# Performance work log

Measured on AMD Instinct MI355X. Metric: run time of the kernel, lower is better.

The kernel has to match this reference:

```python
import jax, jax.numpy as jnp
import numpy as np

B, T, E, H = 2, 2048, 768, 12
DH = E // H  # per-head attention dim
EPS = 1e-5


def setup_inputs() -> dict:
    key = jax.random.key(0)
    ks = jax.random.split(key, 12)
    s = 0.02
    return {
        "x": jax.random.normal(ks[0], (B, T, E), dtype=jnp.float32),
        # stacked per-head projection weights: [H, E, DH], biases [H, DH]
        "Wq": jax.random.normal(ks[1], (H, E, DH), dtype=jnp.float32) * s,
        "bq": jax.random.normal(ks[2], (H, DH), dtype=jnp.float32) * s,
        "Wk": jax.random.normal(ks[3], (H, E, DH), dtype=jnp.float32) * s,
        "bk": jax.random.normal(ks[4], (H, DH), dtype=jnp.float32) * s,
        "Wv": jax.random.normal(ks[5], (H, E, DH), dtype=jnp.float32) * s,
        "bv": jax.random.normal(ks[6], (H, DH), dtype=jnp.float32) * s,
        "Wo": jax.random.normal(ks[7], (E, E), dtype=jnp.float32) * s,
        "bo": jax.random.normal(ks[8], (E,), dtype=jnp.float32) * s,
        "gamma": jnp.ones((E,), dtype=jnp.float32),
        "beta": jnp.zeros((E,), dtype=jnp.float32),
    }


def reference(x, Wq, bq, Wk, bk, Wv, bv, Wo, bo, gamma, beta):
    # per-head projections (heads stacked on axis h)
    q = jnp.einsum("bte,hed->bhtd", x, Wq) + bq[None, :, None, :]
    k = jnp.einsum("bte,hed->bhtd", x, Wk) + bk[None, :, None, :]
    v = jnp.einsum("bte,hed->bhtd", x, Wv) + bv[None, :, None, :]

    scores = jnp.einsum("bhtd,bhsd->bhts", q, k) / jnp.sqrt(jnp.float32(DH))
    causal = jnp.tril(jnp.ones((T, T), dtype=bool))  # True = keep
    scores = jnp.where(causal[None, None], scores, -jnp.inf)
    attn = jax.nn.softmax(scores, axis=-1)
    o = jnp.einsum("bhts,bhsd->bhtd", attn, v)  # [B,H,T,DH]

    # concat heads in head order -> [B,T,E]
    concat = jnp.transpose(o, (0, 2, 1, 3)).reshape(B, T, E)
    proj = concat @ Wo + bo

    # LayerNorm(proj) then residual add
    mu = jnp.mean(proj, axis=-1, keepdims=True)
    var = jnp.mean((proj - mu) ** 2, axis=-1, keepdims=True)
    normed = (proj - mu) * jax.lax.rsqrt(var + EPS) * gamma + beta
    return x + normed
```

## Files before the change

kernel.cpp:

```cpp
#include <hip/hip_runtime.h>
#include <stdint.h>

#define NROWS 4096
#define EMB   768
#define NQKV  2304
#define TSEQ  2048
#define NHEAD 12
#define NBH   24

typedef unsigned short u16;
typedef u16  ushort4v __attribute__((ext_vector_type(4)));
typedef u16  ushort8 __attribute__((ext_vector_type(8)));
typedef __bf16 bf16x8 __attribute__((ext_vector_type(8)));
typedef float f32x4 __attribute__((ext_vector_type(4)));

typedef const __attribute__((address_space(1))) void* gas_ptr;
typedef __attribute__((address_space(3))) void* las_ptr;

__device__ __forceinline__ u16 f2bf(float f) {
  union { float f; uint32_t u; } v; v.f = f;
  uint32_t u = v.u;
  return (u16)((u + 0x7fffu + ((u >> 16) & 1u)) >> 16);
}
__device__ __forceinline__ float bf2f(u16 u) {
  union { uint32_t u; float f; } v; v.u = ((uint32_t)u) << 16;
  return v.f;
}
__device__ __forceinline__ uint32_t cvtpk(float lo, float hi) {
  uint32_t r;
  asm("v_cvt_pk_bf16_f32 %0, %1, %2" : "=v"(r) : "v"(lo), "v"(hi));
  return r;
}

#define VMCNT0 asm volatile("s_waitcnt vmcnt(0)" ::: "memory")
#define LGKM0  asm volatile("s_waitcnt lgkmcnt(0)" ::: "memory")
#define SBAR   __builtin_amdgcn_s_barrier()
#define SCHED0 __builtin_amdgcn_sched_barrier(0)

__global__ void k_zero(uint32_t* cnt) {
  if (threadIdx.x < 8) cnt[threadIdx.x] = 0;
}

__global__ __launch_bounds__(256) void k_pack_x(const float* __restrict__ x, u16* __restrict__ xb) {
  int i = (blockIdx.x * 256 + threadIdx.x) * 8;
  float4 a = *(const float4*)(x + i);
  float4 b = *(const float4*)(x + i + 4);
  uint4 o;
  o.x = cvtpk(a.x, a.y); o.y = cvtpk(a.z, a.w);
  o.z = cvtpk(b.x, b.y); o.w = cvtpk(b.z, b.w);
  *(uint4*)(xb + i) = o;
}

__global__ __launch_bounds__(256) void k_pack_wqkv(const float* __restrict__ Wq, const float* __restrict__ Wk,
                            const float* __restrict__ Wv, const float* __restrict__ bq,
                            const float* __restrict__ bk, const float* __restrict__ bv,
                            u16* __restrict__ wt, float* __restrict__ bias) {
  int idx = blockIdx.x * 256 + threadIdx.x;
  if (idx >= NQKV * EMB) return;
  int n = idx / EMB, e = idx - n * EMB;
  int sel = n / EMB;
  int c = n - sel * EMB;
  int h = c >> 6, d = c & 63;
  const float* W = sel == 0 ? Wq : (sel == 1 ? Wk : Wv);
  wt[idx] = f2bf(W[((size_t)h * EMB + e) * 64 + d]);
  if (e == 0) {
    const float* bs = sel == 0 ? bq : (sel == 1 ? bk : bv);
    bias[n] = bs[h * 64 + d];
  }
}

__global__ __launch_bounds__(256) void k_pack_wo(const float* __restrict__ Wo, u16* __restrict__ wot) {
  int idx = blockIdx.x * 256 + threadIdx.x;
  if (idx >= EMB * EMB) return;
  int n = idx / EMB, e = idx - n * EMB;
  wot[idx] = f2bf(Wo[(size_t)e * EMB + n]);
}

template<int BM, int BN, int OUT_MODE>
__global__ __launch_bounds__(256) void k_gemm(const u16* __restrict__ A, const u16* __restrict__ Bt,
                                              const float* __restrict__ bias, void* __restrict__ Cout,
                                              u16* __restrict__ vtout, int M, int N, int K) {
  constexpr int MR = BM / 32, NR = BN / 32;
  __shared__ u16 lds_a[BM * 64];
  __shared__ u16 lds_b[BN * 64];
  int tid = threadIdx.x;
  int w = tid >> 6, lane = tid & 63;
  int wr = w >> 1, wc = w & 1;
  int m0 = blockIdx.x * BM, n0 = blockIdx.y * BN;
  int lrow = lane & 15, g = lane >> 4;

  f32x4 zero = {0.f, 0.f, 0.f, 0.f};
  f32x4 acc[MR][NR];
  for (int m = 0; m < MR; ++m) for (int n = 0; n < NR; ++n) acc[m][n] = zero;

  int l8 = lane >> 3, c8 = lane & 7;

  for (int k0 = 0; k0 < K; k0 += 64) {
#pragma unroll
    for (int i = 0; i < BM / 32; ++i) {
      int row = w * (BM / 4) + 8 * i + l8;
      int c16 = c8 ^ (row & 7);
      const u16* ga = A + (size_t)(m0 + row) * K + k0 + c16 * 8;
      __builtin_amdgcn_global_load_lds((gas_ptr)ga, (las_ptr)(lds_a + (w * (BM / 4) + 8 * i) * 64), 16, 0, 0);
    }
#pragma unroll
    for (int i = 0; i < BN / 32; ++i) {
      int row = w * (BN / 4) + 8 * i + l8;
      int c16 = c8 ^ (row & 7);
      const u16* gb = Bt + (size_t)(n0 + row) * K + k0 + c16 * 8;
      __builtin_amdgcn_global_load_lds((gas_ptr)gb, (las_ptr)(lds_b + (w * (BN / 4) + 8 * i) * 64), 16, 0, 0);
    }
    __syncthreads();
    bf16x8 af[MR][2], bfr[NR][2];
#pragma unroll
    for (int m = 0; m < MR; ++m)
#pragma unroll
      for (int kc = 0; kc < 2; ++kc) {
        int row = wr * (BM / 2) + m * 16 + lrow;
        int ch = (kc * 4 + g) ^ (row & 7);
        af[m][kc] = *(const bf16x8*)(lds_a + row * 64 + ch * 8);
      }
#pragma unroll
    for (int n = 0; n < NR; ++n)
#pragma unroll
      for (int kc = 0; kc < 2; ++kc) {
        int row = wc * (BN / 2) + n * 16 + lrow;
        int ch = (kc * 4 + g) ^ (row & 7);
        bfr[n][kc] = *(const bf16x8*)(lds_b + row * 64 + ch * 8);
      }
#pragma unroll
    for (int kc = 0; kc < 2; ++kc)
#pragma unroll
      for (int m = 0; m < MR; ++m)
#pragma unroll
        for (int n = 0; n < NR; ++n)
          acc[m][n] = __builtin_amdgcn_mfma_f32_16x16x32_bf16(af[m][kc], bfr[n][kc], acc[m][n], 0, 0, 0);
    __syncthreads();
  }

#pragma unroll
  for (int m = 0; m < MR; ++m)
#pragma unroll
    for (int n = 0; n < NR; ++n) {
      int col = n0 + wc * (BN / 2) + n * 16 + lrow;
      float bcol = bias[col];
      int row0 = m0 + wr * (BM / 2) + m * 16 + 4 * g;
      if (OUT_MODE == 2 && col >= 2 * EMB) {
        int c = col - 2 * EMB;
        int hh = c >> 6, d = c & 63;
        int bb = row0 >> 11, t = row0 & 2047;
        int y = bb * NHEAD + hh;
        ushort4v pk;
#pragma unroll
        for (int r = 0; r < 4; ++r) pk[r] = f2bf(acc[m][n][r] + bcol);
        *(ushort4v*)(vtout + (size_t)(y * 64 + d) * TSEQ + t) = pk;
      } else {
#pragma unroll
        for (int r = 0; r < 4; ++r) {
          int row = row0 + r;
          float v = acc[m][n][r] + bcol;
          if (OUT_MODE == 1) ((float*)Cout)[(size_t)row * N + col] = v;
          else               ((u16*)Cout)[(size_t)row * N + col] = f2bf(v);
        }
      }
    }
}

__global__ __launch_bounds__(256, 4) void k_attn(const u16* __restrict__ qkv, const u16* __restrict__ vt,
                                                 u16* __restrict__ aout, uint32_t* __restrict__ cnt,
                                                 u16* __restrict__ pO, float* __restrict__ pL) {
  __shared__ u16 kbuf[2][64 * 64];
  __shared__ u16 vbuf[2][64 * 64];
  __shared__ u16 pbuf[4][16 * 64];
  __shared__ int task_s;
  int tid = threadIdx.x;
  int w = tid >> 6, lane = tid & 63;
  int ql = lane & 15, g = lane >> 4;
  int xcd = blockIdx.x & 7;
  const float sc2 = 0.18033688f;
  u16* pw = &pbuf[w][0];
  int swz = (ql & 7) << 3;
  int l8 = lane >> 3, c8 = lane & 7;

  for (;;) {
    if (tid == 0) task_s = (int)atomicAdd(&cnt[xcd], 1u);
    __syncthreads();
    int tau = task_s;
    __syncthreads();
    if (tau >= 144) break;

    int rank = tau / 3, yl = tau - rank * 3;
    int qb, t0, t1ex, cslot; bool direct;
    if (rank < 16)       { qb = 16 + rank; t0 = 0;  t1ex = 16;     cslot = 0; direct = false; }
    else if (!(rank & 1)){ int i = (rank - 16) >> 1; qb = 31 - i; t0 = 16; t1ex = qb + 1; cslot = 1; direct = false; }
    else                 { int i = (rank - 16) >> 1; qb = 15 - i; t0 = 0;  t1ex = qb + 1; cslot = 0; direct = true; }

    int y = xcd * 3 + yl;
    int b = y / NHEAD, h = y - b * NHEAD;
    int qrow0w = qb * 64 + w * 16;
    int qg = qrow0w + ql;

    const u16* qp = qkv + (size_t)(b * TSEQ + qg) * NQKV + h * 64;
    bf16x8 bq0 = *(const bf16x8*)(qp + g * 8);
    bf16x8 bq1 = *(const bf16x8*)(qp + 32 + g * 8);

    const u16* kst = qkv + (size_t)(b * TSEQ) * NQKV + EMB + h * 64;
    const u16* vst = vt + (size_t)y * 64 * TSEQ;

    f32x4 zero = {0.f, 0.f, 0.f, 0.f};
    f32x4 o[4]; for (int n = 0; n < 4; ++n) o[n] = zero;
    float lr = 0.f;

    auto STAGE = [&](int bi, int t_) {
#pragma unroll
      for (int i = 0; i < 2; ++i) {
        int row = i * 32 + 8 * w + l8;
        int c16 = c8 ^ (row & 7);
        const u16* gk = kst + (size_t)(t_ * 64 + row) * NQKV + c16 * 8;
        __builtin_amdgcn_global_load_lds((gas_ptr)gk, (las_ptr)(&kbuf[bi][(i * 32 + 8 * w) * 64]), 16, 0, 0);
        const u16* gv = vst + (size_t)row * TSEQ + t_ * 64 + c16 * 8;
        __builtin_amdgcn_global_load_lds((gas_ptr)gv, (las_ptr)(&vbuf[bi][(i * 32 + 8 * w) * 64]), 16, 0, 0);
      }
    };

    STAGE(t0 & 1, t0);
    for (int t = t0; t < t1ex; ++t) {
      int cur = t & 1;
      VMCNT0;
      SBAR;
      if (t + 1 < t1ex) STAGE(cur ^ 1, t + 1);

      const u16* kb = &kbuf[cur][0];
      const u16* vb = &vbuf[cur][0];
      int s0 = t * 64;

      f32x4 st[4];
#pragma unroll
      for (int sblk = 0; sblk < 4; ++sblk) {
        int row = sblk * 16 + ql;
        bf16x8 ka0 = *(const bf16x8*)(kb + ((row * 64 + 8 * g) ^ swz));
        bf16x8 ka1 = *(const bf16x8*)(kb + ((row * 64 + 32 + 8 * g) ^ swz));
        f32x4 acc = zero;
        acc = __builtin_amdgcn_mfma_f32_16x16x32_bf16(ka0, bq0, acc, 0, 0, 0);
        acc = __builtin_amdgcn_mfma_f32_16x16x32_bf16(ka1, bq1, acc, 0, 0, 0);
        st[sblk] = acc;
      }

      bool lastt = (t == qb);
      float e[4][4];
#pragma unroll
      for (int sblk = 0; sblk < 4; ++sblk)
#pragma unroll
        for (int r = 0; r < 4; ++r) {
          float vv = __builtin_fmaf(st[sblk][r], sc2, -2.0f);
          if (lastt) {
            int sg = s0 + sblk * 16 + 4 * g + r;
            if (sg > qg) vv = -1e30f;
          }
          float ee = __builtin_amdgcn_exp2f(vv);
          e[sblk][r] = ee;
          lr += ee;
        }

#pragma unroll
      for (int sblk = 0; sblk < 4; ++sblk) {
        uint2 dw;
        dw.x = cvtpk(e[sblk][0], e[sblk][1]);
        dw.y = cvtpk(e[sblk][2], e[sblk][3]);
        *(uint2*)(pw + ((ql * 64 + sblk * 16 + 4 * g) ^ swz)) = dw;
      }
      LGKM0; SCHED0;
      bf16x8 ap0 = *(const bf16x8*)(pw + ((ql * 64 + 8 * g) ^ swz));
      bf16x8 ap1 = *(const bf16x8*)(pw + ((ql * 64 + 32 + 8 * g) ^ swz));

#pragma unroll
      for (int n = 0; n < 4; ++n) {
        int row = n * 16 + ql;
        bf16x8 vb0 = *(const bf16x8*)(vb + ((row * 64 + 8 * g) ^ swz));
        bf16x8 vb1 = *(const bf16x8*)(vb + ((row * 64 + 32 + 8 * g) ^ swz));
        o[n] = __builtin_amdgcn_mfma_f32_16x16x32_bf16(ap0, vb0, o[n], 0, 0, 0);
        o[n] = __builtin_amdgcn_mfma_f32_16x16x32_bf16(ap1, vb1, o[n], 0, 0, 0);
      }
    }

    float lw = lr;
    lw += __shfl_xor(lw, 16);
    lw += __shfl_xor(lw, 32);

    if (direct) {
      float linv = 1.0f / lw;
      float li[4];
#pragma unroll
      for (int r = 0; r < 4; ++r) li[r] = __shfl(linv, 4 * g + r);
#pragma unroll
      for (int n = 0; n < 4; ++n)
#pragma unroll
        for (int r = 0; r < 4; ++r) {
          int q = qrow0w + 4 * g + r;
          aout[(size_t)(b * TSEQ + q) * EMB + h * 64 + n * 16 + ql] = f2bf(o[n][r] * li[r]);
        }
    } else {
      int blk = y * 16 + (qb - 16);
      u16* po = pO + ((size_t)blk * 2 + cslot) * 4096;
      float* pl = pL + ((size_t)blk * 2 + cslot) * 64;
      if (g == 0) pl[w * 16 + ql] = lw;
#pragma unroll
      for (int n = 0; n < 4; ++n)
#pragma unroll
        for (int r = 0; r < 4; ++r) {
          int qloc = w * 16 + 4 * g + r;
          po[qloc * 64 + n * 16 + ql] = f2bf(o[n][r]);
        }
    }
  }
}

__global__ __launch_bounds__(256) void k_combine(const u16* __restrict__ pO, const float* __restrict__ pL,
                                                 u16* __restrict__ aout) {
  int blk = blockIdx.x;
  int y = blk >> 4, qb = 16 + (blk & 15);
  int b = y / NHEAD, h = y - b * NHEAD;
  int tid = threadIdx.x;
  int row = tid >> 2, c0 = (tid & 3) * 16;
  const u16* p0 = pO + ((size_t)blk * 2) * 4096 + row * 64 + c0;
  const u16* p1 = p0 + 4096;
  float l = pL[blk * 128 + row] + pL[blk * 128 + 64 + row];
  float rinv = 1.0f / l;
  ushort8 a0 = *(const ushort8*)(p0);
  ushort8 a1 = *(const ushort8*)(p0 + 8);
  ushort8 b0 = *(const ushort8*)(p1);
  ushort8 b1 = *(const ushort8*)(p1 + 8);
  ushort8 o0, o1;
#pragma unroll
  for (int j = 0; j < 8; j += 2) {
    uint32_t w0 = cvtpk((bf2f(a0[j]) + bf2f(b0[j])) * rinv, (bf2f(a0[j+1]) + bf2f(b0[j+1])) * rinv);
    o0[j] = (u16)(w0 & 0xffff); o0[j+1] = (u16)(w0 >> 16);
    uint32_t w1 = cvtpk((bf2f(a1[j]) + bf2f(b1[j])) * rinv, (bf2f(a1[j+1]) + bf2f(b1[j+1])) * rinv);
    o1[j] = (u16)(w1 & 0xffff); o1[j+1] = (u16)(w1 >> 16);
  }
  u16* dst = aout + (size_t)(b * TSEQ + qb * 64 + row) * EMB + h * 64 + c0;
  *(ushort8*)dst = o0;
  *(ushort8*)(dst + 8) = o1;
}

__global__ __launch_bounds__(256) void k_ln_res(const float* __restrict__ proj, const float* __restrict__ x,
                                                const float* __restrict__ gamma, const float* __restrict__ beta,
                                                float* __restrict__ out) {
  __shared__ float smem[2][4];
  int row = blockIdx.x;
  const float* pr = proj + (size_t)row * EMB;
  const float* xr = x + (size_t)row * EMB;
  float* orow = out + (size_t)row * EMB;
  int tid = threadIdx.x;
  float v[3];
  float s = 0.f, s2 = 0.f;
#pragma unroll
  for (int i = 0; i < 3; ++i) { v[i] = pr[tid + 256 * i]; s += v[i]; s2 += v[i] * v[i]; }
#pragma unroll
  for (int m = 1; m < 64; m <<= 1) { s += __shfl_xor(s, m); s2 += __shfl_xor(s2, m); }
  int w = tid >> 6, lane = tid & 63;
  if (lane == 0) { smem[0][w] = s; smem[1][w] = s2; }
  __syncthreads();
  s  = smem[0][0] + smem[0][1] + smem[0][2] + smem[0][3];
  s2 = smem[1][0] + smem[1][1] + smem[1][2] + smem[1][3];
  float mu = s * (1.f / EMB);
  float var = s2 * (1.f / EMB) - mu * mu;
  float rstd = rsqrtf(var + 1e-5f);
#pragma unroll
  for (int i = 0; i < 3; ++i) {
    int c = tid + 256 * i;
    orow[c] = xr[c] + (v[i] - mu) * rstd * gamma[c] + beta[c];
  }
}

extern "C" void kernel_launch(void* const* d_in, const int* in_sizes, int n_in,
                              void* d_out, int out_size, void* d_ws, size_t ws_size,
                              hipStream_t stream) {
  const float* x     = (const float*)d_in[0];
  const float* Wq    = (const float*)d_in[1];
  const float* bq    = (const float*)d_in[2];
  const float* Wk    = (const float*)d_in[3];
  const float* bk    = (const float*)d_in[4];
  const float* Wv    = (const float*)d_in[5];
  const float* bv    = (const float*)d_in[6];
  const float* Wo    = (const float*)d_in[7];
  const float* bo    = (const float*)d_in[8];
  const float* gamma = (const float*)d_in[9];
  const float* beta  = (const float*)d_in[10];
  float* out = (float*)d_out;

  char* ws = (char*)d_ws;
  size_t off = 0;
  u16* xb    = (u16*)(ws + off); off += (size_t)NROWS * EMB * 2;
  u16* wqkvt = (u16*)(ws + off); off += (size_t)NQKV * EMB * 2;
  u16* wot   = (u16*)(ws + off); off += (size_t)EMB * EMB * 2;
  float* bqkv = (float*)(ws + off); off += (size_t)NQKV * 4;
  uint32_t* cnt = (uint32_t*)(ws + off); off += 64;
  u16* qkv   = (u16*)(ws + off); off += (size_t)NROWS * NQKV * 2;
  u16* vt    = (u16*)(ws + off); off += (size_t)NBH * 64 * TSEQ * 2;
  u16* aout  = (u16*)(ws + off); off += (size_t)NROWS * EMB * 2;
  u16* pO    = (u16*)(ws + off); off += (size_t)NBH * 16 * 2 * 4096 * 2;
  float* pL  = (float*)(ws + off); off += (size_t)NBH * 16 * 2 * 64 * 4;
  float* proj = (float*)qkv;

  k_zero<<<1, 64, 0, stream>>>(cnt);
  k_pack_x<<<NROWS * EMB / (256 * 8), 256, 0, stream>>>(x, xb);
  k_pack_wqkv<<<(NQKV * EMB + 255) / 256, 256, 0, stream>>>(Wq, Wk, Wv, bq, bk, bv, wqkvt, bqkv);
  k_pack_wo<<<(EMB * EMB + 255) / 256, 256, 0, stream>>>(Wo, wot);
  k_gemm<128, 128, 2><<<dim3(NROWS / 128, NQKV / 128), 256, 0, stream>>>(xb, wqkvt, bqkv, qkv, vt, NROWS, NQKV, EMB);
  k_attn<<<dim3(1024), 256, 0, stream>>>(qkv, vt, aout, cnt, pO, pL);
  k_combine<<<dim3(NBH * 16), 256, 0, stream>>>(pO, pL, aout);
  k_gemm<128, 64, 1><<<dim3(NROWS / 128, EMB / 64), 256, 0, stream>>>(aout, wot, bo, proj, nullptr, NROWS, EMB, EMB);
  k_ln_res<<<NROWS, 256, 0, stream>>>(proj, x, gamma, beta, out);
}
```

Baseline: 137.1 us.

## Merge pack kernels into one launch with LDS-tiled weight transposes

Replaces the zero, x-pack, Wqkv-pack and Wo-pack kernels with a single launch whose block ranges handle each job. The weight transposes now go through a 64x64 LDS tile, so global reads and writes are coalesced instead of strided. The QKV bias is read directly from bq/bk/bv in the GEMM epilogue, which removes the packed bias buffer. Attention occupancy is also lowered to 3 blocks/SM with a 768-block persistent grid, which may change latency hiding.

```diff
diff --git a/kernel.cpp b/kernel.cpp
--- a/kernel.cpp
+++ b/kernel.cpp
@@ -37,48 +37,77 @@
 #define SBAR   __builtin_amdgcn_s_barrier()
 #define SCHED0 __builtin_amdgcn_sched_barrier(0)
 
-__global__ void k_zero(uint32_t* cnt) {
-  if (threadIdx.x < 8) cnt[threadIdx.x] = 0;
-}
-
-__global__ __launch_bounds__(256) void k_pack_x(const float* __restrict__ x, u16* __restrict__ xb) {
-  int i = (blockIdx.x * 256 + threadIdx.x) * 8;
-  float4 a = *(const float4*)(x + i);
-  float4 b = *(const float4*)(x + i + 4);
-  uint4 o;
-  o.x = cvtpk(a.x, a.y); o.y = cvtpk(a.z, a.w);
-  o.z = cvtpk(b.x, b.y); o.w = cvtpk(b.z, b.w);
-  *(uint4*)(xb + i) = o;
-}
-
-__global__ __launch_bounds__(256) void k_pack_wqkv(const float* __restrict__ Wq, const float* __restrict__ Wk,
-                            const float* __restrict__ Wv, const float* __restrict__ bq,
-                            const float* __restrict__ bk, const float* __restrict__ bv,
-                            u16* __restrict__ wt, float* __restrict__ bias) {
-  int idx = blockIdx.x * 256 + threadIdx.x;
-  if (idx >= NQKV * EMB) return;
-  int n = idx / EMB, e = idx - n * EMB;
-  int sel = n / EMB;
-  int c = n - sel * EMB;
-  int h = c >> 6, d = c & 63;
-  const float* W = sel == 0 ? Wq : (sel == 1 ? Wk : Wv);
-  wt[idx] = f2bf(W[((size_t)h * EMB + e) * 64 + d]);
-  if (e == 0) {
-    const float* bs = sel == 0 ? bq : (sel == 1 ? bk : bv);
-    bias[n] = bs[h * 64 + d];
-  }
-}
-
-__global__ __launch_bounds__(256) void k_pack_wo(const float* __restrict__ Wo, u16* __restrict__ wot) {
-  int idx = blockIdx.x * 256 + threadIdx.x;
-  if (idx >= EMB * EMB) return;
-  int n = idx / EMB, e = idx - n * EMB;
-  wot[idx] = f2bf(Wo[(size_t)e * EMB + n]);
+__global__ __launch_bounds__(256) void k_pack(const float* __restrict__ x, u16* __restrict__ xb,
+                                              const float* __restrict__ Wq, const float* __restrict__ Wk,
+                                              const float* __restrict__ Wv, u16* __restrict__ wt,
+                                              const float* __restrict__ Wo, u16* __restrict__ wot,
+                                              uint32_t* __restrict__ cnt) {
+  int bid = blockIdx.x, tid = threadIdx.x;
+  if (bid == 0 && tid < 8) cnt[tid] = 0;
+  if (bid < 1536) {
+    int i = bid * 2048 + tid * 8;
+    float4 a = *(const float4*)(x + i);
+    float4 b = *(const float4*)(x + i + 4);
+    uint4 o;
+    o.x = cvtpk(a.x, a.y); o.y = cvtpk(a.z, a.w);
+    o.z = cvtpk(b.x, b.y); o.w = cvtpk(b.z, b.w);
+    *(uint4*)(xb + i) = o;
+    return;
+  }
+  __shared__ u16 lds[64][68];
+  if (bid < 1968) {
+    int t = bid - 1536;
+    int sel = t / 144, rest = t - sel * 144;
+    int h = rest / 12, ec = rest - h * 12;
+    const float* W = sel == 0 ? Wq : (sel == 1 ? Wk : Wv);
+    const float* src = W + ((size_t)(h * EMB + ec * 64) * 64);
+    int e = tid >> 2, d0 = (tid & 3) * 16;
+#pragma unroll
+    for (int j = 0; j < 4; ++j) {
+      float4 v = *(const float4*)(src + (size_t)e * 64 + d0 + 4 * j);
+      ushort4v pk;
+      uint32_t w0 = cvtpk(v.x, v.y), w1 = cvtpk(v.z, v.w);
+      pk[0] = (u16)(w0 & 0xffff); pk[1] = (u16)(w0 >> 16);
+      pk[2] = (u16)(w1 & 0xffff); pk[3] = (u16)(w1 >> 16);
+      *(ushort4v*)(&lds[e][d0 + 4 * j]) = pk;
+    }
+    __syncthreads();
+    int d = tid >> 2, e0 = (tid & 3) * 16;
+    ushort8 o0, o1;
+#pragma unroll
+    for (int j = 0; j < 8; ++j) { o0[j] = lds[e0 + j][d]; o1[j] = lds[e0 + 8 + j][d]; }
+    int n = sel * EMB + h * 64 + d;
+    u16* dst = wt + (size_t)n * EMB + ec * 64 + e0;
+    *(ushort8*)dst = o0;
+    *(ushort8*)(dst + 8) = o1;
+  } else {
+    int t = bid - 1968;
+    int er = t / 12, nc = t - er * 12;
+    int e = tid >> 2, n0 = (tid & 3) * 16;
+#pragma unroll
+    for (int j = 0; j < 4; ++j) {
+      float4 v = *(const float4*)(Wo + (size_t)(er * 64 + e) * EMB + nc * 64 + n0 + 4 * j);
+      ushort4v pk;
+      uint32_t w0 = cvtpk(v.x, v.y), w1 = cvtpk(v.z, v.w);
+      pk[0] = (u16)(w0 & 0xffff); pk[1] = (u16)(w0 >> 16);
+      pk[2] = (u16)(w1 & 0xffff); pk[3] = (u16)(w1 >> 16);
+      *(ushort4v*)(&lds[e][n0 + 4 * j]) = pk;
+    }
+    __syncthreads();
+    int n = tid >> 2, e0 = (tid & 3) * 16;
+    ushort8 o0, o1;
+#pragma unroll
+    for (int j = 0; j < 8; ++j) { o0[j] = lds[e0 + j][n]; o1[j] = lds[e0 + 8 + j][n]; }
+    u16* dst = wot + (size_t)(nc * 64 + n) * EMB + er * 64 + e0;
+    *(ushort8*)dst = o0;
+    *(ushort8*)(dst + 8) = o1;
+  }
 }
 
 template<int BM, int BN, int OUT_MODE>
 __global__ __launch_bounds__(256) void k_gemm(const u16* __restrict__ A, const u16* __restrict__ Bt,
-                                              const float* __restrict__ bias, void* __restrict__ Cout,
+                                              const float* __restrict__ b0, const float* __restrict__ b1,
+                                              const float* __restrict__ b2, void* __restrict__ Cout,
                                               u16* __restrict__ vtout, int M, int N, int K) {
   constexpr int MR = BM / 32, NR = BN / 32;
   __shared__ u16 lds_a[BM * 64];
@@ -143,7 +172,13 @@
 #pragma unroll
     for (int n = 0; n < NR; ++n) {
       int col = n0 + wc * (BN / 2) + n * 16 + lrow;
-      float bcol = bias[col];
+      float bcol;
+      if (OUT_MODE == 1) bcol = b0[col];
+      else {
+        int sel = col >= 1536 ? 2 : (col >= 768 ? 1 : 0);
+        const float* bs = sel == 0 ? b0 : (sel == 1 ? b1 : b2);
+        bcol = bs[col - sel * EMB];
+      }
       int row0 = m0 + wr * (BM / 2) + m * 16 + 4 * g;
       if (OUT_MODE == 2 && col >= 2 * EMB) {
         int c = col - 2 * EMB;
@@ -166,7 +201,7 @@
     }
 }
 
-__global__ __launch_bounds__(256, 4) void k_attn(const u16* __restrict__ qkv, const u16* __restrict__ vt,
+__global__ __launch_bounds__(256, 3) void k_attn(const u16* __restrict__ qkv, const u16* __restrict__ vt,
                                                  u16* __restrict__ aout, uint32_t* __restrict__ cnt,
                                                  u16* __restrict__ pO, float* __restrict__ pL) {
   __shared__ u16 kbuf[2][64 * 64];
@@ -394,7 +429,6 @@
   u16* xb    = (u16*)(ws + off); off += (size_t)NROWS * EMB * 2;
   u16* wqkvt = (u16*)(ws + off); off += (size_t)NQKV * EMB * 2;
   u16* wot   = (u16*)(ws + off); off += (size_t)EMB * EMB * 2;
-  float* bqkv = (float*)(ws + off); off += (size_t)NQKV * 4;
   uint32_t* cnt = (uint32_t*)(ws + off); off += 64;
   u16* qkv   = (u16*)(ws + off); off += (size_t)NROWS * NQKV * 2;
   u16* vt    = (u16*)(ws + off); off += (size_t)NBH * 64 * TSEQ * 2;
@@ -403,13 +437,10 @@
   float* pL  = (float*)(ws + off); off += (size_t)NBH * 16 * 2 * 64 * 4;
   float* proj = (float*)qkv;
 
-  k_zero<<<1, 64, 0, stream>>>(cnt);
-  k_pack_x<<<NROWS * EMB / (256 * 8), 256, 0, stream>>>(x, xb);
-  k_pack_wqkv<<<(NQKV * EMB + 255) / 256, 256, 0, stream>>>(Wq, Wk, Wv, bq, bk, bv, wqkvt, bqkv);
-  k_pack_wo<<<(EMB * EMB + 255) / 256, 256, 0, stream>>>(Wo, wot);
-  k_gemm<128, 128, 2><<<dim3(NROWS / 128, NQKV / 128), 256, 0, stream>>>(xb, wqkvt, bqkv, qkv, vt, NROWS, NQKV, EMB);
-  k_attn<<<dim3(1024), 256, 0, stream>>>(qkv, vt, aout, cnt, pO, pL);
+  k_pack<<<dim3(2112), 256, 0, stream>>>(x, xb, Wq, Wk, Wv, wqkvt, Wo, wot, cnt);
+  k_gemm<128, 128, 2><<<dim3(NROWS / 128, NQKV / 128), 256, 0, stream>>>(xb, wqkvt, bq, bk, bv, qkv, vt, NROWS, NQKV, EMB);
+  k_attn<<<dim3(768), 256, 0, stream>>>(qkv, vt, aout, cnt, pO, pL);
   k_combine<<<dim3(NBH * 16), 256, 0, stream>>>(pO, pL, aout);
-  k_gemm<128, 64, 1><<<dim3(NROWS / 128, EMB / 64), 256, 0, stream>>>(aout, wot, bo, proj, nullptr, NROWS, EMB, EMB);
+  k_gemm<128, 64, 1><<<dim3(NROWS / 128, EMB / 64), 256, 0, stream>>>(aout, wot, bo, nullptr, nullptr, proj, nullptr, NROWS, EMB, EMB);
   k_ln_res<<<NROWS, 256, 0, stream>>>(proj, x, gamma, beta, out);
 }
```

Result: faster. 114.5 us (-16.5%).
